# Optimization experiments

Hardware: AMD Instinct MI355X
Metric: run time of the kernel (lower is better)

Reference implementation:

```python
import jax, jax.numpy as jnp
import numpy as np

DIM = 512
NUM_HEADS = 8
HEAD_DIM = DIM // NUM_HEADS
B, N = 2, 4096


def setup_inputs() -> dict:
    key = jax.random.key(0)
    k1, k2, k3, k4, k5 = jax.random.split(key, 5)
    s = 1.0 / np.sqrt(DIM)
    return {
        "x": jax.random.normal(k1, (B, N, DIM), dtype=jnp.float32),
        "w_qkv": jax.random.normal(k2, (DIM, 3 * DIM), dtype=jnp.float32) * s,
        "b_qkv": jax.random.normal(k3, (3 * DIM,), dtype=jnp.float32) * 0.01,
        "w_proj": jax.random.normal(k4, (DIM, DIM), dtype=jnp.float32) * s,
        "b_proj": jax.random.normal(k5, (DIM,), dtype=jnp.float32) * 0.01,
    }


def reference(x, w_qkv, b_qkv, w_proj, b_proj):
    b, n, c = x.shape
    h, d = NUM_HEADS, HEAD_DIM
    qkv = x @ w_qkv + b_qkv                      # [B,N,3C]
    q, k, v = jnp.split(qkv, 3, axis=-1)
    # [B,N,C] -> [B,H,N,D]
    q = q.reshape(b, n, h, d).transpose(0, 2, 1, 3)
    k = k.reshape(b, n, h, d).transpose(0, 2, 1, 3)
    v = v.reshape(b, n, h, d).transpose(0, 2, 1, 3)
    scale = d ** (-0.5)
    attn = jnp.einsum('bhqd,bhkd->bhqk', q, k) * scale  # [B,H,N,N]
    attn = jax.nn.softmax(attn, axis=-1)
    out = jnp.einsum('bhqk,bhkd->bhqd', attn, v)        # [B,H,N,D]
    out = out.transpose(0, 2, 1, 3).reshape(b, n, c)
    return out @ w_proj + b_proj
```

## Files before the change

kernel.cpp:

```cpp
#include <hip/hip_runtime.h>

#define DIM_C 512
#define HEADS 8
#define HD 64
#define BATCH 2
#define SEQ 4096
#define QSCALE (0.125f * 1.44269504088896f)

typedef __attribute__((ext_vector_type(8))) short short8;
typedef __attribute__((ext_vector_type(4))) float f32x4;

__device__ __forceinline__ ushort f2bf(float f) {
    union { float f; unsigned u; } x; x.f = f;
    unsigned r = x.u + 0x7fffu + ((x.u >> 16) & 1u);
    return (ushort)(r >> 16);
}

__device__ __forceinline__ void gl_lds16(const void* g, void* l) {
    __builtin_amdgcn_global_load_lds(
        (const __attribute__((address_space(1))) unsigned int*)g,
        (__attribute__((address_space(3))) unsigned int*)l, 16, 0, 0);
}

__device__ __forceinline__ unsigned cvt_pk_bf16(float lo, float hi) {
    unsigned w;
    asm("v_cvt_pk_bf16_f32 %0, %1, %2" : "=v"(w) : "v"(lo), "v"(hi));
    return w;
}

__global__ __launch_bounds__(256)
void convert_bf16(const float* __restrict__ in, ushort* __restrict__ out, int n4) {
    int i = blockIdx.x * blockDim.x + threadIdx.x;
    const int stride = gridDim.x * blockDim.x;
    for (; i < n4; i += stride) {
        const float4 v = reinterpret_cast<const float4*>(in)[i];
        ushort4 o;
        o.x = f2bf(v.x); o.y = f2bf(v.y); o.z = f2bf(v.z); o.w = f2bf(v.w);
        reinterpret_cast<ushort4*>(out)[i] = o;
    }
}

__global__ __launch_bounds__(256)
void transpose_w_bf16(const float* __restrict__ in, ushort* __restrict__ out,
                      int R, int C) {
    __shared__ ushort Ls[64 * 68];
    const int tid = threadIdx.x;
    const int c0 = blockIdx.x * 64, r0 = blockIdx.y * 64;
    #pragma unroll
    for (int p = 0; p < 4; ++p) {
        const int idx = tid + p * 256;
        const int r = idx >> 4, c4 = (idx & 15) * 4;
        const float4 v = *reinterpret_cast<const float4*>(
            &in[(size_t)(r0 + r) * C + c0 + c4]);
        ushort4 o; o.x = f2bf(v.x); o.y = f2bf(v.y); o.z = f2bf(v.z); o.w = f2bf(v.w);
        *reinterpret_cast<ushort4*>(&Ls[r * 68 + c4]) = o;
    }
    __syncthreads();
    #pragma unroll
    for (int p = 0; p < 4; ++p) {
        const int idx = tid + p * 256;
        const int c = idx >> 4, r4 = (idx & 15) * 4;
        ushort4 o;
        o.x = Ls[(r4 + 0) * 68 + c]; o.y = Ls[(r4 + 1) * 68 + c];
        o.z = Ls[(r4 + 2) * 68 + c]; o.w = Ls[(r4 + 3) * 68 + c];
        *reinterpret_cast<ushort4*>(&out[(size_t)(c0 + c) * R + r0 + r4]) = o;
    }
}

__global__ __launch_bounds__(256)
void transpose_v(const ushort* __restrict__ qkvb, ushort* __restrict__ vt) {
    __shared__ ushort Ls[64 * 68];
    const int tid = threadIdx.x;
    const int n0 = blockIdx.x * 64;
    const int bh = blockIdx.y, b = bh >> 3, h = bh & 7;
    #pragma unroll
    for (int p = 0; p < 4; ++p) {
        const int idx = tid + p * 256;
        const int r = idx >> 4, c4 = (idx & 15) * 4;
        const ushort4 v = *reinterpret_cast<const ushort4*>(
            &qkvb[(size_t)(b * SEQ + n0 + r) * 1536 + 1024 + h * 64 + c4]);
        *reinterpret_cast<ushort4*>(&Ls[r * 68 + c4]) = v;
    }
    __syncthreads();
    #pragma unroll
    for (int p = 0; p < 4; ++p) {
        const int idx = tid + p * 256;
        const int d = idx >> 4, n4 = (idx & 15) * 4;
        ushort4 o;
        o.x = Ls[(n4 + 0) * 68 + d]; o.y = Ls[(n4 + 1) * 68 + d];
        o.z = Ls[(n4 + 2) * 68 + d]; o.w = Ls[(n4 + 3) * 68 + d];
        *reinterpret_cast<ushort4*>(&vt[((size_t)bh * 64 + d) * SEQ + n0 + n4]) = o;
    }
}

template<int MODE>
__global__ __launch_bounds__(256)
void gemm_mfma(const ushort* __restrict__ A, const ushort* __restrict__ BT,
               const float* __restrict__ bias, void* __restrict__ Cout,
               int M, int N, int K) {
    __shared__ ushort As[128 * 64];
    __shared__ ushort Bs[128 * 64];
    const int tid = threadIdx.x;
    const int lane = tid & 63, wid = tid >> 6;
    const int lr = lane & 15, lg = lane >> 4;
    const int wm = wid >> 1, wn = wid & 1;
    const int rowBase = blockIdx.y * 128, colBase = blockIdx.x * 128;
    const int l8 = lane >> 3;
    const int lchunk = (lane & 7) ^ l8;

    f32x4 acc[4][4];
    #pragma unroll
    for (int i = 0; i < 4; ++i)
        #pragma unroll
        for (int j = 0; j < 4; ++j)
            #pragma unroll
            for (int c = 0; c < 4; ++c) acc[i][j][c] = 0.f;

    for (int k0 = 0; k0 < K; k0 += 64) {
        #pragma unroll
        for (int i = 0; i < 4; ++i) {
            const int r = wid * 32 + i * 8;
            gl_lds16(&A[(size_t)(rowBase + r + l8) * K + k0 + lchunk * 8],
                     &As[r * 64]);
            gl_lds16(&BT[(size_t)(colBase + r + l8) * K + k0 + lchunk * 8],
                     &Bs[r * 64]);
        }
        __syncthreads();
        #pragma unroll
        for (int s = 0; s < 2; ++s) {
            short8 af[4], bf[4];
            #pragma unroll
            for (int mt = 0; mt < 4; ++mt) {
                const int r = wm * 64 + mt * 16 + lr;
                af[mt] = *reinterpret_cast<const short8*>(
                    &As[r * 64 + ((s * 4 + lg) ^ (r & 7)) * 8]);
            }
            #pragma unroll
            for (int nt = 0; nt < 4; ++nt) {
                const int r = wn * 64 + nt * 16 + lr;
                bf[nt] = *reinterpret_cast<const short8*>(
                    &Bs[r * 64 + ((s * 4 + lg) ^ (r & 7)) * 8]);
            }
            #pragma unroll
            for (int mt = 0; mt < 4; ++mt)
                #pragma unroll
                for (int nt = 0; nt < 4; ++nt)
                    acc[mt][nt] = __builtin_amdgcn_mfma_f32_16x16x32_bf16(
                        af[mt], bf[nt], acc[mt][nt], 0, 0, 0);
        }
        __syncthreads();
    }

    #pragma unroll
    for (int nt = 0; nt < 4; ++nt) {
        const int col = colBase + wn * 64 + nt * 16 + lr;
        const float bv = bias[col];
        const float qs = (MODE == 1 && col < DIM_C) ? QSCALE : 1.f;
        #pragma unroll
        for (int mt = 0; mt < 4; ++mt) {
            #pragma unroll
            for (int j = 0; j < 4; ++j) {
                const int row = rowBase + wm * 64 + mt * 16 + lg * 4 + j;
                const float v = (acc[mt][nt][j] + bv) * qs;
                if (MODE == 0)
                    reinterpret_cast<float*>(Cout)[(size_t)row * N + col] = v;
                else
                    reinterpret_cast<ushort*>(Cout)[(size_t)row * N + col] = f2bf(v);
            }
        }
    }
}

__global__ __launch_bounds__(512)
void flash_attn8(const ushort* __restrict__ qkvb, const ushort* __restrict__ vt,
                 ushort* __restrict__ aoutb) {
    __shared__ ushort Ks[2][128 * 64];
    __shared__ ushort Vs[2][64 * 128];
    __shared__ ushort Ps[8 * 16 * 64];

    const int tid = threadIdx.x;
    const int lane = tid & 63, wid = tid >> 6;
    const int lr = lane & 15, lg = lane >> 4;
    const int qt = blockIdx.x, bh = blockIdx.y;
    const int b = bh >> 3, h = bh & 7;
    const int q0 = qt * 128;
    const int l8 = lane >> 3;
    const int lchunk = (lane & 7) ^ l8;
    const int rsw = (lr & 7) ^ ((lr >> 3) << 2);

    short8 onesf;
    #pragma unroll
    for (int i = 0; i < 8; ++i) onesf[i] = (short)0x3F80;

    short8 qf[2];
    {
        const size_t qrow = (size_t)b * SEQ + q0 + wid * 16 + lr;
        #pragma unroll
        for (int s = 0; s < 2; ++s)
            qf[s] = *reinterpret_cast<const short8*>(
                &qkvb[qrow * 1536 + h * 64 + s * 32 + lg * 8]);
    }

    float m = -1e30f;
    f32x4 lacc;
    lacc[0] = 0.f; lacc[1] = 0.f; lacc[2] = 0.f; lacc[3] = 0.f;
    f32x4 oa[4];
    #pragma unroll
    for (int dt = 0; dt < 4; ++dt)
        #pragma unroll
        for (int c = 0; c < 4; ++c) oa[dt][c] = 0.f;

    auto stage = [&](int kt, int buf) {
        const int k0 = kt * 128;
        #pragma unroll
        for (int i = 0; i < 2; ++i) {
            const int r = wid * 16 + i * 8;
            gl_lds16(&qkvb[(size_t)(b * SEQ + k0 + r + l8) * 1536 + DIM_C +
                           h * 64 + lchunk * 8],
                     &Ks[buf][r * 64]);
        }
        #pragma unroll
        for (int i = 0; i < 2; ++i) {
            const int d0 = wid * 8 + i * 4;
            const int d = d0 + (lane >> 4);
            const int c16 = lane & 15;
            const int gch = (c16 & 8) | ((c16 & 7) ^ (d & 7));
            gl_lds16(&vt[((size_t)bh * 64 + d) * SEQ + k0 + gch * 8],
                     &Vs[buf][d0 * 128]);
        }
    };

    stage(0, 0);
    const int NT = SEQ / 128;
    for (int kt = 0; kt < NT; ++kt) {
        const int buf = kt & 1;
        __syncthreads();
        if (kt + 1 < NT) stage(kt + 1, buf ^ 1);

        f32x4 sa[8];
        #pragma unroll
        for (int t = 0; t < 8; ++t)
            #pragma unroll
            for (int c = 0; c < 4; ++c) sa[t][c] = 0.f;
        __builtin_amdgcn_s_setprio(1);
        #pragma unroll
        for (int t = 0; t < 8; ++t) {
            const int n = t * 16 + lr;
            #pragma unroll
            for (int s = 0; s < 2; ++s) {
                const short8 kf = *reinterpret_cast<const short8*>(
                    &Ks[buf][n * 64 + ((s * 4 + lg) ^ (n & 7)) * 8]);
                sa[t] = __builtin_amdgcn_mfma_f32_16x16x32_bf16(
                    kf, qf[s], sa[t], 0, 0, 0);
            }
        }
        __builtin_amdgcn_s_setprio(0);

        float mx = fmaxf(fmaxf(sa[0][0], sa[0][1]), sa[0][2]);
        #pragma unroll
        for (int t = 1; t < 8; ++t)
            mx = fmaxf(fmaxf(mx, sa[t][0]),
                       fmaxf(fmaxf(sa[t][1], sa[t][2]), sa[t][3]));
        mx = fmaxf(mx, sa[0][3]);
        mx = fmaxf(mx, __shfl_xor(mx, 16));
        mx = fmaxf(mx, __shfl_xor(mx, 32));
        if (__any(mx > m + 8.f)) {
            const float mnew = fmaxf(m, mx);
            const float alpha = exp2f(m - mnew);
            m = mnew;
            lacc[0] *= alpha; lacc[1] *= alpha;
            lacc[2] *= alpha; lacc[3] *= alpha;
            const float a0 = __shfl(alpha, lg * 4 + 0);
            const float a1 = __shfl(alpha, lg * 4 + 1);
            const float a2 = __shfl(alpha, lg * 4 + 2);
            const float a3 = __shfl(alpha, lg * 4 + 3);
            #pragma unroll
            for (int dt = 0; dt < 4; ++dt) {
                oa[dt][0] *= a0; oa[dt][1] *= a1;
                oa[dt][2] *= a2; oa[dt][3] *= a3;
            }
        }
        #pragma unroll
        for (int t = 0; t < 8; ++t)
            #pragma unroll
            for (int r = 0; r < 4; ++r)
                sa[t][r] = exp2f(sa[t][r] - m);

        const int pb = wid * (16 * 64);
        const int pbase = pb + lr * 64 + (lg & 1) * 4;
        #pragma unroll
        for (int kh = 0; kh < 2; ++kh) {
            #pragma unroll
            for (int t = 0; t < 4; ++t) {
                const int chunk = (2 * t + (lg >> 1)) ^ rsw;
                uint2 w;
                w.x = cvt_pk_bf16(sa[kh * 4 + t][0], sa[kh * 4 + t][1]);
                w.y = cvt_pk_bf16(sa[kh * 4 + t][2], sa[kh * 4 + t][3]);
                *reinterpret_cast<uint2*>(&Ps[pbase + chunk * 8]) = w;
            }
            short8 pf[2];
            #pragma unroll
            for (int s = 0; s < 2; ++s)
                pf[s] = *reinterpret_cast<const short8*>(
                    &Ps[pb + lr * 64 + ((lg + 4 * s) ^ rsw) * 8]);

            __builtin_amdgcn_s_setprio(1);
            #pragma unroll
            for (int s = 0; s < 2; ++s)
                lacc = __builtin_amdgcn_mfma_f32_16x16x32_bf16(
                    onesf, pf[s], lacc, 0, 0, 0);
            #pragma unroll
            for (int dt = 0; dt < 4; ++dt) {
                const int d = dt * 16 + lr;
                #pragma unroll
                for (int s = 0; s < 2; ++s) {
                    const short8 vf = *reinterpret_cast<const short8*>(
                        &Vs[buf][d * 128 +
                                 (kh * 8 + ((s * 4 + lg) ^ (d & 7))) * 8]);
                    oa[dt] = __builtin_amdgcn_mfma_f32_16x16x32_bf16(
                        pf[s], vf, oa[dt], 0, 0, 0);
                }
            }
            __builtin_amdgcn_s_setprio(0);
        }
    }

    const float linv = 1.f / lacc[0];
    const float v0 = __shfl(linv, lg * 4 + 0);
    const float v1 = __shfl(linv, lg * 4 + 1);
    const float v2 = __shfl(linv, lg * 4 + 2);
    const float v3 = __shfl(linv, lg * 4 + 3);
    const size_t orow0 = (size_t)b * SEQ + q0 + wid * 16;
    #pragma unroll
    for (int dt = 0; dt < 4; ++dt) {
        const int c = h * HD + dt * 16 + lr;
        aoutb[(orow0 + lg * 4 + 0) * DIM_C + c] = f2bf(oa[dt][0] * v0);
        aoutb[(orow0 + lg * 4 + 1) * DIM_C + c] = f2bf(oa[dt][1] * v1);
        aoutb[(orow0 + lg * 4 + 2) * DIM_C + c] = f2bf(oa[dt][2] * v2);
        aoutb[(orow0 + lg * 4 + 3) * DIM_C + c] = f2bf(oa[dt][3] * v3);
    }
}

extern "C" void kernel_launch(void* const* d_in, const int* in_sizes, int n_in,
                              void* d_out, int out_size, void* d_ws, size_t ws_size,
                              hipStream_t stream) {
    const float* x      = (const float*)d_in[0];
    const float* w_qkv  = (const float*)d_in[1];
    const float* b_qkv  = (const float*)d_in[2];
    const float* w_proj = (const float*)d_in[3];
    const float* b_proj = (const float*)d_in[4];
    float* out = (float*)d_out;

    const int M = BATCH * SEQ;
    ushort* xb     = (ushort*)d_ws;
    ushort* wqkvT  = xb     + (size_t)M * DIM_C;
    ushort* wprojT = wqkvT  + (size_t)3 * DIM_C * DIM_C;
    ushort* qkvb   = wprojT + (size_t)DIM_C * DIM_C;
    ushort* vt     = qkvb   + (size_t)M * 3 * DIM_C;
    ushort* aoutb  = vt     + (size_t)16 * HD * SEQ;

    convert_bf16<<<2048, 256, 0, stream>>>(x, xb, M * DIM_C / 4);
    transpose_w_bf16<<<dim3(3 * DIM_C / 64, DIM_C / 64), 256, 0, stream>>>(
        w_qkv, wqkvT, DIM_C, 3 * DIM_C);
    transpose_w_bf16<<<dim3(DIM_C / 64, DIM_C / 64), 256, 0, stream>>>(
        w_proj, wprojT, DIM_C, DIM_C);

    gemm_mfma<1><<<dim3(3 * DIM_C / 128, M / 128), 256, 0, stream>>>(
        xb, wqkvT, b_qkv, qkvb, M, 3 * DIM_C, DIM_C);

    transpose_v<<<dim3(SEQ / 64, BATCH * HEADS), 256, 0, stream>>>(qkvb, vt);

    flash_attn8<<<dim3(SEQ / 128, BATCH * HEADS), 512, 0, stream>>>(
        qkvb, vt, aoutb);

    gemm_mfma<0><<<dim3(DIM_C / 128, M / 128), 256, 0, stream>>>(
        aoutb, wprojT, b_proj, out, M, DIM_C, DIM_C);
}
```

Baseline: 243.0 us.

## Remap GEMM and attention blocks per XCD and fuse the prep kernels into one

Both GEMMs and the attention kernel now launch on a 1D grid. Block ids are remapped so that consecutive work tiles (the same head's query tiles, or neighbouring GEMM tiles) land on the same XCD, which should improve L2 reuse of shared K/V and weight data. The x conversion and the two weight transposes are merged into one launch to save launch overhead. The row-swizzle term for attention LDS accesses is also simplified, which may change bank-conflict behaviour.

```diff
diff --git a/kernel.cpp b/kernel.cpp
--- a/kernel.cpp
+++ b/kernel.cpp
@@ -28,24 +28,14 @@
     return w;
 }
 
-__global__ __launch_bounds__(256)
-void convert_bf16(const float* __restrict__ in, ushort* __restrict__ out, int n4) {
-    int i = blockIdx.x * blockDim.x + threadIdx.x;
-    const int stride = gridDim.x * blockDim.x;
-    for (; i < n4; i += stride) {
-        const float4 v = reinterpret_cast<const float4*>(in)[i];
-        ushort4 o;
-        o.x = f2bf(v.x); o.y = f2bf(v.y); o.z = f2bf(v.z); o.w = f2bf(v.w);
-        reinterpret_cast<ushort4*>(out)[i] = o;
-    }
-}
-
-__global__ __launch_bounds__(256)
-void transpose_w_bf16(const float* __restrict__ in, ushort* __restrict__ out,
-                      int R, int C) {
-    __shared__ ushort Ls[64 * 68];
-    const int tid = threadIdx.x;
-    const int c0 = blockIdx.x * 64, r0 = blockIdx.y * 64;
+__device__ __forceinline__ int xcd_swz(int j, int nb) {
+    return (j & 7) * (nb >> 3) + (j >> 3);
+}
+
+__device__ __forceinline__ void tw_body(const float* __restrict__ in,
+                                        ushort* __restrict__ out,
+                                        ushort* Ls, int R, int C,
+                                        int c0, int r0, int tid) {
     #pragma unroll
     for (int p = 0; p < 4; ++p) {
         const int idx = tid + p * 256;
@@ -64,6 +54,31 @@
         o.x = Ls[(r4 + 0) * 68 + c]; o.y = Ls[(r4 + 1) * 68 + c];
         o.z = Ls[(r4 + 2) * 68 + c]; o.w = Ls[(r4 + 3) * 68 + c];
         *reinterpret_cast<ushort4*>(&out[(size_t)(c0 + c) * R + r0 + r4]) = o;
+    }
+}
+
+__global__ __launch_bounds__(256)
+void prep_fused(const float* __restrict__ x, ushort* __restrict__ xb,
+                const float* __restrict__ w_qkv, ushort* __restrict__ wqkvT,
+                const float* __restrict__ w_proj, ushort* __restrict__ wprojT,
+                int n4) {
+    __shared__ ushort Ls[64 * 68];
+    const int j = blockIdx.x;
+    const int tid = threadIdx.x;
+    if (j < 192) {
+        tw_body(w_qkv, wqkvT, Ls, 512, 1536, (j % 24) * 64, (j / 24) * 64, tid);
+    } else if (j < 256) {
+        const int jj = j - 192;
+        tw_body(w_proj, wprojT, Ls, 512, 512, (jj % 8) * 64, (jj / 8) * 64, tid);
+    } else {
+        int i = (j - 256) * 256 + tid;
+        const int stride = 2048 * 256;
+        for (; i < n4; i += stride) {
+            const float4 v = reinterpret_cast<const float4*>(x)[i];
+            ushort4 o;
+            o.x = f2bf(v.x); o.y = f2bf(v.y); o.z = f2bf(v.z); o.w = f2bf(v.w);
+            reinterpret_cast<ushort4*>(xb)[i] = o;
+        }
     }
 }
 
@@ -104,7 +119,9 @@
     const int lane = tid & 63, wid = tid >> 6;
     const int lr = lane & 15, lg = lane >> 4;
     const int wm = wid >> 1, wn = wid & 1;
-    const int rowBase = blockIdx.y * 128, colBase = blockIdx.x * 128;
+    const int nbx = N >> 7;
+    const int wgid = xcd_swz(blockIdx.x, gridDim.x);
+    const int rowBase = (wgid / nbx) * 128, colBase = (wgid % nbx) * 128;
     const int l8 = lane >> 3;
     const int lchunk = (lane & 7) ^ l8;
 
@@ -181,12 +198,13 @@
     const int tid = threadIdx.x;
     const int lane = tid & 63, wid = tid >> 6;
     const int lr = lane & 15, lg = lane >> 4;
-    const int qt = blockIdx.x, bh = blockIdx.y;
+    const int wgid = xcd_swz(blockIdx.x, gridDim.x);
+    const int qt = wgid & 31, bh = wgid >> 5;
     const int b = bh >> 3, h = bh & 7;
     const int q0 = qt * 128;
     const int l8 = lane >> 3;
     const int lchunk = (lane & 7) ^ l8;
-    const int rsw = (lr & 7) ^ ((lr >> 3) << 2);
+    const int rsw = lr & 7;
 
     short8 onesf;
     #pragma unroll
@@ -359,20 +377,17 @@
     ushort* vt     = qkvb   + (size_t)M * 3 * DIM_C;
     ushort* aoutb  = vt     + (size_t)16 * HD * SEQ;
 
-    convert_bf16<<<2048, 256, 0, stream>>>(x, xb, M * DIM_C / 4);
-    transpose_w_bf16<<<dim3(3 * DIM_C / 64, DIM_C / 64), 256, 0, stream>>>(
-        w_qkv, wqkvT, DIM_C, 3 * DIM_C);
-    transpose_w_bf16<<<dim3(DIM_C / 64, DIM_C / 64), 256, 0, stream>>>(
-        w_proj, wprojT, DIM_C, DIM_C);
-
-    gemm_mfma<1><<<dim3(3 * DIM_C / 128, M / 128), 256, 0, stream>>>(
+    prep_fused<<<2304, 256, 0, stream>>>(x, xb, w_qkv, wqkvT, w_proj, wprojT,
+                                         M * DIM_C / 4);
+
+    gemm_mfma<1><<<(3 * DIM_C / 128) * (M / 128), 256, 0, stream>>>(
         xb, wqkvT, b_qkv, qkvb, M, 3 * DIM_C, DIM_C);
 
     transpose_v<<<dim3(SEQ / 64, BATCH * HEADS), 256, 0, stream>>>(qkvb, vt);
 
-    flash_attn8<<<dim3(SEQ / 128, BATCH * HEADS), 512, 0, stream>>>(
+    flash_attn8<<<(SEQ / 128) * (BATCH * HEADS), 512, 0, stream>>>(
         qkvb, vt, aoutb);
 
-    gemm_mfma<0><<<dim3(DIM_C / 128, M / 128), 256, 0, stream>>>(
+    gemm_mfma<0><<<(DIM_C / 128) * (M / 128), 256, 0, stream>>>(
         aoutb, wprojT, b_proj, out, M, DIM_C, DIM_C);
 }
```

Measured after the change: 235.9 us. -2.9%, faster.
